# Kernel optimization log

Hardware: AMD Instinct MI355X
Metric: run time of the kernel (lower is better)

Reference implementation:

```python
import jax, jax.numpy as jnp
import numpy as np

B, S, D_MODEL, HEAD_DIM = 8, 2048, 2048, 128
NEG = -1.0e9

def setup_inputs() -> dict:
    key = jax.random.key(0)
    ks = jax.random.split(key, 7)
    scale = 1.0 / np.sqrt(D_MODEL)
    return {
        "hidden_state": jax.random.normal(ks[0], (B, S, D_MODEL), dtype=jnp.float32),
        "Wq": jax.random.normal(ks[1], (D_MODEL, HEAD_DIM), dtype=jnp.float32) * scale,
        "bq": jnp.zeros((HEAD_DIM,), dtype=jnp.float32),
        "Wk": jax.random.normal(ks[2], (D_MODEL, HEAD_DIM), dtype=jnp.float32) * scale,
        "bk": jnp.zeros((HEAD_DIM,), dtype=jnp.float32),
        "Wv": jax.random.normal(ks[3], (D_MODEL, HEAD_DIM), dtype=jnp.float32) * scale,
        "bv": jnp.zeros((HEAD_DIM,), dtype=jnp.float32),
    }

def reference(hidden_state, Wq, bq, Wk, bk, Wv, bv):
    # Projections: [B,S,D] @ [D,H] -> [B,S,H]
    q = hidden_state @ Wq + bq
    k = hidden_state @ Wk + bk
    v = hidden_state @ Wv + bv
    # Scaled dot-product scores: [B,S,S]
    scores = jnp.einsum('bqh,bkh->bqk', q, k) / jnp.sqrt(jnp.float32(HEAD_DIM))
    # Causal mask: strictly-upper-triangular (diagonal kept) gets -1e9, matching
    # band_part(upper) - band_part(diag) in the original.
    S_len = q.shape[1]
    row = jnp.arange(S_len)[:, None]
    col = jnp.arange(S_len)[None, :]
    mask = jnp.where(col > row, jnp.float32(NEG), jnp.float32(0.0))
    scores = scores + mask
    weights = jax.nn.softmax(scores, axis=-1)
    return jnp.einsum('bqk,bkh->bqh', weights, v)
```

## Files before the change

kernel.cpp:

```cpp
#include <hip/hip_runtime.h>
#include <hip/hip_bf16.h>
#include <stdint.h>

#define B_DIM 8
#define S_LEN 2048
#define DMODEL 2048
#define HDIM 128

typedef __attribute__((ext_vector_type(4))) float f32x4;
typedef __attribute__((ext_vector_type(8))) short bf16x8;
typedef __attribute__((ext_vector_type(4))) short bf16x4;
typedef __attribute__((ext_vector_type(4))) unsigned int u32x4;
typedef unsigned short u16;
typedef unsigned int u32;

__device__ __forceinline__ u16 f2bf(float f) {
    union { float f; u32 u; } v; v.f = f;
    u32 u = v.u;
    u32 r = (u + 0x7fffu + ((u >> 16) & 1u)) >> 16;
    return (u16)r;
}

__device__ __forceinline__ u32 pk2bf(float a, float b) {
    float2 f2; f2.x = a; f2.y = b;
    __hip_bfloat162 h = __float22bfloat162_rn(f2);
    union { __hip_bfloat162 h; u32 u; } cv; cv.h = h;
    return cv.u;
}

__device__ __forceinline__ void async_copy16(u16* lds, const u16* g) {
    __builtin_amdgcn_global_load_lds((const __attribute__((address_space(1))) u32*)g,
                                     (__attribute__((address_space(3))) u32*)lds,
                                     16, 0, 0);
}

__global__ void pack_weights(const float* __restrict__ Wq, const float* __restrict__ Wk,
                             const float* __restrict__ Wv, u16* __restrict__ Wp) {
    __shared__ u16 tl[64 * 64];
    int t = threadIdx.x;
    int bx = blockIdx.x;
    int w = bx >> 6;
    int kt = (bx >> 1) & 31;
    int ht = bx & 1;
    int k0 = kt * 64, h0 = ht * 64;
    const float* W = (w == 0) ? Wq : ((w == 1) ? Wk : Wv);

    int kl = t >> 2, hc = t & 3;
    const float* src = W + (size_t)(k0 + kl) * HDIM + h0 + hc * 16;
#pragma unroll
    for (int half = 0; half < 2; half++) {
        bf16x8 p;
#pragma unroll
        for (int j = 0; j < 8; j++) p[j] = (short)f2bf(src[half * 8 + j]);
        int slot = hc * 2 + half;
        *(bf16x8*)((char*)tl + kl * 128 + ((slot ^ (kl & 7)) << 4)) = p;
    }
    __syncthreads();
    int hl = t >> 2, kc = t & 3;
    u16* dst = Wp + (size_t)(w * HDIM + h0 + hl) * DMODEL + k0 + kc * 16;
#pragma unroll
    for (int half = 0; half < 2; half++) {
        bf16x8 p;
#pragma unroll
        for (int j = 0; j < 8; j++) {
            int k = kc * 16 + half * 8 + j;
            p[j] = *(u16*)((char*)tl + k * 128 + (((hl >> 3) ^ (k & 7)) << 4) + (hl & 7) * 2);
        }
        *(bf16x8*)(dst + half * 8) = p;
    }
}

__launch_bounds__(512)
__global__ void qkv_gemm(const float* __restrict__ hs, const u16* __restrict__ Wp,
                         const float* __restrict__ bq, const float* __restrict__ bk,
                         const float* __restrict__ bv,
                         u16* __restrict__ Qb, u16* __restrict__ Kb, u16* __restrict__ Vt) {
    __shared__ u16 As[2][64 * 64];
    __shared__ u16 Bs[2][384 * 64];

    int t = threadIdx.x;
    int wv = t >> 6, l = t & 63, lr = l & 15, lq = l >> 4;
    int wm = wv >> 2, wn = wv & 3;
    int m0 = blockIdx.x * 64;
    int ko = ((blockIdx.x >> 3) & 31) << 6;

#define KW(X) (((X) + ko) & (DMODEL - 1))

    f32x4 acc[2][6] = {};

    int ar = t >> 3, aq = t & 7;
    const float* gA = hs + (size_t)(m0 + ar) * DMODEL + aq * 8;

    f32x4 p0A, p1A, p0B, p1B;

#define STAGE_B(K0, BUF)                                                    \
    {                                                                       \
        _Pragma("unroll")                                                   \
        for (int i = 0; i < 6; i++) {                                       \
            int c = i * 512 + t;                                            \
            int n = c >> 3, s = c & 7;                                      \
            async_copy16(&Bs[BUF][c * 8],                                   \
                         Wp + (size_t)n * DMODEL + (K0) + ((s ^ (n & 7)) * 8)); \
        }                                                                   \
    }
#define WRITE_A(BUF, V0, V1)                                                \
    {                                                                       \
        u32x4 pk;                                                           \
        pk.x = pk2bf(V0[0], V0[1]); pk.y = pk2bf(V0[2], V0[3]);             \
        pk.z = pk2bf(V1[0], V1[1]); pk.w = pk2bf(V1[2], V1[3]);             \
        *(u32x4*)((char*)&As[BUF][0] + ar * 128 + ((aq ^ (ar & 7)) << 4)) = pk; \
    }
#define COMPUTE(CUR)                                                        \
    {                                                                       \
        _Pragma("unroll")                                                   \
        for (int kk = 0; kk < 2; kk++) {                                    \
            bf16x8 afr[2], bfr[6];                                          \
            int slot = kk * 4 + lq;                                         \
            _Pragma("unroll")                                               \
            for (int mi = 0; mi < 2; mi++) {                                \
                int row = wm * 32 + mi * 16 + lr;                           \
                afr[mi] = *(bf16x8*)((char*)&As[CUR][0] + row * 128 + ((slot ^ (row & 7)) << 4)); \
            }                                                               \
            _Pragma("unroll")                                               \
            for (int ni = 0; ni < 6; ni++) {                                \
                int row = wn * 96 + ni * 16 + lr;                           \
                bfr[ni] = *(bf16x8*)((char*)&Bs[CUR][0] + row * 128 + ((slot ^ (row & 7)) << 4)); \
            }                                                               \
            __builtin_amdgcn_s_setprio(1);                                  \
            _Pragma("unroll")                                               \
            for (int mi = 0; mi < 2; mi++)                                  \
                _Pragma("unroll")                                           \
                for (int ni = 0; ni < 6; ni++)                              \
                    acc[mi][ni] = __builtin_amdgcn_mfma_f32_16x16x32_bf16(afr[mi], bfr[ni], acc[mi][ni], 0, 0, 0); \
            __builtin_amdgcn_s_setprio(0);                                  \
        }                                                                   \
    }
#define SYNC_PIPE                                                           \
    asm volatile("s_waitcnt vmcnt(2) lgkmcnt(0)" ::: "memory");             \
    __builtin_amdgcn_sched_barrier(0);                                      \
    __builtin_amdgcn_s_barrier();                                           \
    __builtin_amdgcn_sched_barrier(0);

    p0A = *(const f32x4*)(gA + KW(0)); p1A = *(const f32x4*)(gA + KW(0) + 4);
    STAGE_B(KW(0), 0);
    WRITE_A(0, p0A, p1A);
    p0A = *(const f32x4*)(gA + KW(64)); p1A = *(const f32x4*)(gA + KW(64) + 4);
    __syncthreads();

    for (int k0 = 0; k0 < DMODEL; k0 += 128) {
        {
            int ks = KW(k0 + 64);
            int kp = KW(k0 + 128);
            STAGE_B(ks, 1);
            p0B = *(const f32x4*)(gA + kp); p1B = *(const f32x4*)(gA + kp + 4);
            COMPUTE(0);
            WRITE_A(1, p0A, p1A);
            SYNC_PIPE
        }
        {
            int ks = KW(k0 + 128);
            int kp = KW(k0 + 192);
            STAGE_B(ks, 0);
            p0A = *(const f32x4*)(gA + kp); p1A = *(const f32x4*)(gA + kp + 4);
            COMPUTE(1);
            WRITE_A(0, p0B, p1B);
            SYNC_PIPE
        }
    }

#pragma unroll
    for (int ni = 0; ni < 6; ni++) {
        int col = wn * 96 + ni * 16 + lr;
        int w = col >> 7, h = col & 127;
        const float* bp = (w == 0) ? bq : ((w == 1) ? bk : bv);
        float bias = bp[h];
#pragma unroll
        for (int mi = 0; mi < 2; mi++) {
            int row0 = m0 + wm * 32 + mi * 16 + lq * 4;
            if (w == 2) {
                int b = row0 >> 11, s0 = row0 & (S_LEN - 1);
                bf16x4 pv;
#pragma unroll
                for (int r = 0; r < 4; r++) pv[r] = (short)f2bf(acc[mi][ni][r] + bias);
                *(bf16x4*)(Vt + (size_t)(b * HDIM + h) * S_LEN + s0) = pv;
            } else {
                float scale = (w == 0) ? 0.08838834764831845f : 1.0f;
                u16* dst = (w == 0) ? Qb : Kb;
#pragma unroll
                for (int r = 0; r < 4; r++)
                    dst[(size_t)(row0 + r) * HDIM + h] = f2bf((acc[mi][ni][r] + bias) * scale);
            }
        }
    }
#undef STAGE_B
#undef WRITE_A
#undef COMPUTE
#undef SYNC_PIPE
#undef KW
}

__launch_bounds__(256, 2)
__global__ void attn(const u16* __restrict__ Qb, const u16* __restrict__ Kb,
                     const u16* __restrict__ Vt, float* __restrict__ out) {
    __shared__ char lds[66560];
    float* Om = (float*)lds;
    float* ml = (float*)(lds + 65536);

    int t = threadIdx.x;
    int wv = t >> 6, l = t & 63, lr = l & 15, lq = l >> 4;
    int bx = blockIdx.x;
    int b = bx & 7;
    int qt = 63 - (bx >> 3);
    int qr0 = qt * 32;
    size_t qbase = (size_t)b * S_LEN;
    char* Pw = lds + wv * 16384;

    bf16x8 aqf[2][4];
#pragma unroll
    for (int mi = 0; mi < 2; mi++)
#pragma unroll
        for (int kk = 0; kk < 4; kk++)
            aqf[mi][kk] = *(const bf16x8*)(Qb + (qbase + qr0 + mi * 16 + lr) * HDIM + kk * 32 + lq * 8);

    f32x4 o_acc[2][8] = {};
    float m_run[2][4], l_run[2][4];
#pragma unroll
    for (int mi = 0; mi < 2; mi++)
#pragma unroll
        for (int r = 0; r < 4; r++) { m_run[mi][r] = -1e38f; l_run[mi][r] = 0.f; }

    int ktd = qt >> 1;
    const u16* Kbase = Kb + qbase * HDIM;
    const u16* Vbase = Vt + (size_t)b * HDIM * S_LEN;

    int cnt = (ktd >= wv) ? (((ktd - wv) >> 2) + 1) : 0;

    for (int j = 0; j < cnt; ++j) {
        int kt = wv + (j << 2);
        int kv0 = kt * 64;

        f32x4 sa[2][4] = {};
#pragma unroll
        for (int kk = 0; kk < 4; kk++) {
            bf16x8 bk8[4];
#pragma unroll
            for (int n = 0; n < 4; n++)
                bk8[n] = *(const bf16x8*)(Kbase + (size_t)(kv0 + n * 16 + lr) * HDIM + kk * 32 + lq * 8);
            __builtin_amdgcn_s_setprio(1);
#pragma unroll
            for (int n = 0; n < 4; n++) {
                sa[0][n] = __builtin_amdgcn_mfma_f32_16x16x32_bf16(aqf[0][kk], bk8[n], sa[0][n], 0, 0, 0);
                sa[1][n] = __builtin_amdgcn_mfma_f32_16x16x32_bf16(aqf[1][kk], bk8[n], sa[1][n], 0, 0, 0);
            }
            __builtin_amdgcn_s_setprio(0);
        }

        if (kt == ktd) {
#pragma unroll
            for (int n = 0; n < 4; n++) {
                int col = kv0 + n * 16 + lr;
#pragma unroll
                for (int mi = 0; mi < 2; mi++)
#pragma unroll
                    for (int r = 0; r < 4; r++) {
                        int row = qr0 + mi * 16 + lq * 4 + r;
                        if (col > row) sa[mi][n][r] = -1e30f;
                    }
            }
        }

#pragma unroll
        for (int mi = 0; mi < 2; mi++) {
#pragma unroll
            for (int r = 0; r < 4; r++) {
                float pmx = fmaxf(fmaxf(sa[mi][0][r], sa[mi][1][r]), fmaxf(sa[mi][2][r], sa[mi][3][r]));
                if (__any(pmx > m_run[mi][r] + 8.0f)) {
                    float mx = pmx;
#pragma unroll
                    for (int off = 8; off >= 1; off >>= 1) mx = fmaxf(mx, __shfl_xor(mx, off, 64));
                    float mnew = fmaxf(m_run[mi][r], mx);
                    float f = __expf(m_run[mi][r] - mnew);
                    l_run[mi][r] *= f;
                    m_run[mi][r] = mnew;
#pragma unroll
                    for (int n = 0; n < 8; n++) o_acc[mi][n][r] *= f;
                }
                int prow = mi * 16 + lq * 4 + r;
                char* pb = Pw + prow * 128;
#pragma unroll
                for (int n = 0; n < 4; n++) {
                    float e = __expf(sa[mi][n][r] - m_run[mi][r]);
                    l_run[mi][r] += e;
                    int col = n * 16 + lr;
                    *(u16*)(pb + (((col >> 3) ^ (prow & 7)) << 4) + (col & 7) * 2) = f2bf(e);
                }
            }
        }

#pragma unroll
        for (int kk = 0; kk < 2; kk++) {
            int slot = kk * 4 + lq;
            int row0 = lr, row1 = 16 + lr;
            bf16x8 pa0 = *(bf16x8*)(Pw + row0 * 128 + ((slot ^ (row0 & 7)) << 4));
            bf16x8 pa1 = *(bf16x8*)(Pw + row1 * 128 + ((slot ^ (row1 & 7)) << 4));
            __builtin_amdgcn_s_setprio(1);
#pragma unroll
            for (int n = 0; n < 8; n++) {
                bf16x8 vb8 = *(const bf16x8*)(Vbase + (size_t)(n * 16 + lr) * S_LEN + kv0 + kk * 32 + lq * 8);
                o_acc[0][n] = __builtin_amdgcn_mfma_f32_16x16x32_bf16(pa0, vb8, o_acc[0][n], 0, 0, 0);
                o_acc[1][n] = __builtin_amdgcn_mfma_f32_16x16x32_bf16(pa1, vb8, o_acc[1][n], 0, 0, 0);
            }
            __builtin_amdgcn_s_setprio(0);
        }
    }

#pragma unroll
    for (int mi = 0; mi < 2; mi++)
#pragma unroll
        for (int r = 0; r < 4; r++) {
#pragma unroll
            for (int off = 8; off >= 1; off >>= 1)
                l_run[mi][r] += __shfl_xor(l_run[mi][r], off, 64);
        }

    __builtin_amdgcn_sched_barrier(0);
#pragma unroll
    for (int mi = 0; mi < 2; mi++)
#pragma unroll
        for (int n = 0; n < 8; n++)
#pragma unroll
            for (int r = 0; r < 4; r++)
                Om[wv * 4096 + (mi * 16 + lq * 4 + r) * 128 + n * 16 + lr] = o_acc[mi][n][r];
    if (lr == 0) {
#pragma unroll
        for (int mi = 0; mi < 2; mi++)
#pragma unroll
            for (int r = 0; r < 4; r++) {
                int row = mi * 16 + lq * 4 + r;
                ml[wv * 64 + row * 2 + 0] = m_run[mi][r];
                ml[wv * 64 + row * 2 + 1] = l_run[mi][r];
            }
    }
    __syncthreads();

    {
        int row = t >> 3, c0 = (t & 7) * 16;
        float m4[4], l4[4];
#pragma unroll
        for (int w = 0; w < 4; w++) {
            m4[w] = ml[w * 64 + row * 2 + 0];
            l4[w] = ml[w * 64 + row * 2 + 1];
        }
        float ms = fmaxf(fmaxf(m4[0], m4[1]), fmaxf(m4[2], m4[3]));
        float wt[4], ls = 0.f;
#pragma unroll
        for (int w = 0; w < 4; w++) { wt[w] = __expf(m4[w] - ms); ls += l4[w] * wt[w]; }
        float inv = 1.0f / ls;
        f32x4 r0 = (f32x4)0.f, r1 = (f32x4)0.f, r2 = (f32x4)0.f, r3 = (f32x4)0.f;
#pragma unroll
        for (int w = 0; w < 4; w++) {
            const f32x4* Op = (const f32x4*)(Om + w * 4096 + row * 128 + c0);
            r0 += Op[0] * wt[w];
            r1 += Op[1] * wt[w];
            r2 += Op[2] * wt[w];
            r3 += Op[3] * wt[w];
        }
        f32x4* dst = (f32x4*)(out + (qbase + qr0 + row) * HDIM + c0);
        dst[0] = r0 * inv;
        dst[1] = r1 * inv;
        dst[2] = r2 * inv;
        dst[3] = r3 * inv;
    }
}

extern "C" void kernel_launch(void* const* d_in, const int* in_sizes, int n_in,
                              void* d_out, int out_size, void* d_ws, size_t ws_size,
                              hipStream_t stream) {
    const float* hs = (const float*)d_in[0];
    const float* Wq = (const float*)d_in[1];
    const float* bq = (const float*)d_in[2];
    const float* Wk = (const float*)d_in[3];
    const float* bk = (const float*)d_in[4];
    const float* Wv = (const float*)d_in[5];
    const float* bv = (const float*)d_in[6];
    float* out = (float*)d_out;

    char* ws = (char*)d_ws;
    u16* Qb = (u16*)(ws);
    u16* Kb = (u16*)(ws + (size_t)(4  << 20));
    u16* Vt = (u16*)(ws + (size_t)(8  << 20));
    u16* Wp = (u16*)(ws + (size_t)(12 << 20));

    hipLaunchKernelGGL(pack_weights, dim3(192), dim3(256), 0, stream, Wq, Wk, Wv, Wp);
    hipLaunchKernelGGL(qkv_gemm, dim3(256), dim3(512), 0, stream, hs, Wp, bq, bk, bv, Qb, Kb, Vt);
    hipLaunchKernelGGL(attn, dim3(512), dim3(256), 0, stream, Qb, Kb, Vt, out);
}
```

Before: 108.2 us.

## Split QKV GEMM columns across two blocks and use a triple-buffered pipeline

The QKV projection GEMM now splits its 384 output columns into two 192-column halves, so twice as many blocks are launched (512 instead of 256), each with half the B tile and accumulators. The main loop moves from double to triple buffering: it prefetches two stages ahead with finer-grained vmcnt waits and one barrier per 64-wide K step. The goal is better occupancy across the CUs and more overlap of global loads with MFMA work. The cost is that each block reloads and converts the fp32 hidden-state A tile, so total A traffic and conversion work double.

```diff
diff --git a/kernel.cpp b/kernel.cpp
--- a/kernel.cpp
+++ b/kernel.cpp
@@ -75,102 +75,110 @@
                          const float* __restrict__ bq, const float* __restrict__ bk,
                          const float* __restrict__ bv,
                          u16* __restrict__ Qb, u16* __restrict__ Kb, u16* __restrict__ Vt) {
-    __shared__ u16 As[2][64 * 64];
-    __shared__ u16 Bs[2][384 * 64];
+    __shared__ u16 As[3][64 * 64];
+    __shared__ u16 Bs[3][192 * 64];
 
     int t = threadIdx.x;
     int wv = t >> 6, l = t & 63, lr = l & 15, lq = l >> 4;
     int wm = wv >> 2, wn = wv & 3;
-    int m0 = blockIdx.x * 64;
+    int m0 = (blockIdx.x >> 1) * 64;
+    int col0 = (blockIdx.x & 1) * 192;
     int ko = ((blockIdx.x >> 3) & 31) << 6;
 
 #define KW(X) (((X) + ko) & (DMODEL - 1))
 
-    f32x4 acc[2][6] = {};
+    f32x4 acc[2][3] = {};
 
     int ar = t >> 3, aq = t & 7;
     const float* gA = hs + (size_t)(m0 + ar) * DMODEL + aq * 8;
 
-    f32x4 p0A, p1A, p0B, p1B;
+    f32x4 a0[3], a1[3];
 
 #define STAGE_B(K0, BUF)                                                    \
     {                                                                       \
         _Pragma("unroll")                                                   \
-        for (int i = 0; i < 6; i++) {                                       \
+        for (int i = 0; i < 3; i++) {                                       \
             int c = i * 512 + t;                                            \
             int n = c >> 3, s = c & 7;                                      \
             async_copy16(&Bs[BUF][c * 8],                                   \
-                         Wp + (size_t)n * DMODEL + (K0) + ((s ^ (n & 7)) * 8)); \
+                         Wp + (size_t)(col0 + n) * DMODEL + (K0) + ((s ^ (n & 7)) * 8)); \
         }                                                                   \
     }
-#define WRITE_A(BUF, V0, V1)                                                \
+#define LOAD_A(SET, K)                                                      \
+    { a0[SET] = *(const f32x4*)(gA + (K)); a1[SET] = *(const f32x4*)(gA + (K) + 4); }
+#define WRITE_A(BUF, SET)                                                   \
     {                                                                       \
         u32x4 pk;                                                           \
-        pk.x = pk2bf(V0[0], V0[1]); pk.y = pk2bf(V0[2], V0[3]);             \
-        pk.z = pk2bf(V1[0], V1[1]); pk.w = pk2bf(V1[2], V1[3]);             \
+        pk.x = pk2bf(a0[SET][0], a0[SET][1]); pk.y = pk2bf(a0[SET][2], a0[SET][3]); \
+        pk.z = pk2bf(a1[SET][0], a1[SET][1]); pk.w = pk2bf(a1[SET][2], a1[SET][3]); \
         *(u32x4*)((char*)&As[BUF][0] + ar * 128 + ((aq ^ (ar & 7)) << 4)) = pk; \
     }
-#define COMPUTE(CUR)                                                        \
+#define COMPUTE(J)                                                          \
     {                                                                       \
         _Pragma("unroll")                                                   \
         for (int kk = 0; kk < 2; kk++) {                                    \
-            bf16x8 afr[2], bfr[6];                                          \
+            bf16x8 afr[2], bfr[3];                                          \
             int slot = kk * 4 + lq;                                         \
             _Pragma("unroll")                                               \
             for (int mi = 0; mi < 2; mi++) {                                \
                 int row = wm * 32 + mi * 16 + lr;                           \
-                afr[mi] = *(bf16x8*)((char*)&As[CUR][0] + row * 128 + ((slot ^ (row & 7)) << 4)); \
+                afr[mi] = *(bf16x8*)((char*)&As[J][0] + row * 128 + ((slot ^ (row & 7)) << 4)); \
             }                                                               \
             _Pragma("unroll")                                               \
-            for (int ni = 0; ni < 6; ni++) {                                \
-                int row = wn * 96 + ni * 16 + lr;                           \
-                bfr[ni] = *(bf16x8*)((char*)&Bs[CUR][0] + row * 128 + ((slot ^ (row & 7)) << 4)); \
+            for (int ni = 0; ni < 3; ni++) {                                \
+                int row = wn * 48 + ni * 16 + lr;                           \
+                bfr[ni] = *(bf16x8*)((char*)&Bs[J][0] + row * 128 + ((slot ^ (row & 7)) << 4)); \
             }                                                               \
             __builtin_amdgcn_s_setprio(1);                                  \
             _Pragma("unroll")                                               \
             for (int mi = 0; mi < 2; mi++)                                  \
                 _Pragma("unroll")                                           \
-                for (int ni = 0; ni < 6; ni++)                              \
+                for (int ni = 0; ni < 3; ni++)                              \
                     acc[mi][ni] = __builtin_amdgcn_mfma_f32_16x16x32_bf16(afr[mi], bfr[ni], acc[mi][ni], 0, 0, 0); \
             __builtin_amdgcn_s_setprio(0);                                  \
         }                                                                   \
     }
-#define SYNC_PIPE                                                           \
-    asm volatile("s_waitcnt vmcnt(2) lgkmcnt(0)" ::: "memory");             \
-    __builtin_amdgcn_sched_barrier(0);                                      \
-    __builtin_amdgcn_s_barrier();                                           \
+#define QPHASE(J, K0)                                                       \
+    {                                                                       \
+        int kN = KW((K0) + ((J) + 2) * 64);                                 \
+        STAGE_B(kN, ((J) + 2) % 3);                                         \
+        LOAD_A(((J) + 2) % 3, kN);                                          \
+        __builtin_amdgcn_sched_barrier(0);                                  \
+        asm volatile("s_waitcnt vmcnt(5)" ::: "memory");                    \
+        __builtin_amdgcn_sched_barrier(0);                                  \
+        COMPUTE(J);                                                         \
+        WRITE_A(((J) + 1) % 3, ((J) + 1) % 3);                              \
+        asm volatile("s_waitcnt lgkmcnt(0)" ::: "memory");                  \
+        __builtin_amdgcn_sched_barrier(0);                                  \
+        __builtin_amdgcn_s_barrier();                                       \
+        __builtin_amdgcn_sched_barrier(0);                                  \
+    }
+
+    STAGE_B(KW(0), 0);
+    LOAD_A(0, KW(0));
+    STAGE_B(KW(64), 1);
+    LOAD_A(1, KW(64));
     __builtin_amdgcn_sched_barrier(0);
-
-    p0A = *(const f32x4*)(gA + KW(0)); p1A = *(const f32x4*)(gA + KW(0) + 4);
-    STAGE_B(KW(0), 0);
-    WRITE_A(0, p0A, p1A);
-    p0A = *(const f32x4*)(gA + KW(64)); p1A = *(const f32x4*)(gA + KW(64) + 4);
-    __syncthreads();
-
-    for (int k0 = 0; k0 < DMODEL; k0 += 128) {
-        {
-            int ks = KW(k0 + 64);
-            int kp = KW(k0 + 128);
-            STAGE_B(ks, 1);
-            p0B = *(const f32x4*)(gA + kp); p1B = *(const f32x4*)(gA + kp + 4);
-            COMPUTE(0);
-            WRITE_A(1, p0A, p1A);
-            SYNC_PIPE
-        }
-        {
-            int ks = KW(k0 + 128);
-            int kp = KW(k0 + 192);
-            STAGE_B(ks, 0);
-            p0A = *(const f32x4*)(gA + kp); p1A = *(const f32x4*)(gA + kp + 4);
-            COMPUTE(1);
-            WRITE_A(0, p0B, p1B);
-            SYNC_PIPE
-        }
-    }
-
-#pragma unroll
-    for (int ni = 0; ni < 6; ni++) {
-        int col = wn * 96 + ni * 16 + lr;
+    asm volatile("s_waitcnt vmcnt(5)" ::: "memory");
+    __builtin_amdgcn_sched_barrier(0);
+    WRITE_A(0, 0);
+    asm volatile("s_waitcnt lgkmcnt(0)" ::: "memory");
+    __builtin_amdgcn_sched_barrier(0);
+    __builtin_amdgcn_s_barrier();
+    __builtin_amdgcn_sched_barrier(0);
+
+    for (int it = 0; it < 10; ++it) {
+        int kb = it * 192;
+        QPHASE(0, kb)
+        QPHASE(1, kb)
+        QPHASE(2, kb)
+    }
+    QPHASE(0, 1920)
+    QPHASE(1, 1920)
+
+#pragma unroll
+    for (int ni = 0; ni < 3; ni++) {
+        int col = col0 + wn * 48 + ni * 16 + lr;
         int w = col >> 7, h = col & 127;
         const float* bp = (w == 0) ? bq : ((w == 1) ? bk : bv);
         float bias = bp[h];
@@ -193,9 +201,10 @@
         }
     }
 #undef STAGE_B
+#undef LOAD_A
 #undef WRITE_A
 #undef COMPUTE
-#undef SYNC_PIPE
+#undef QPHASE
 #undef KW
 }
 
@@ -392,6 +401,6 @@
     u16* Wp = (u16*)(ws + (size_t)(12 << 20));
 
     hipLaunchKernelGGL(pack_weights, dim3(192), dim3(256), 0, stream, Wq, Wk, Wv, Wp);
-    hipLaunchKernelGGL(qkv_gemm, dim3(256), dim3(512), 0, stream, hs, Wp, bq, bk, bv, Qb, Kb, Vt);
+    hipLaunchKernelGGL(qkv_gemm, dim3(512), dim3(512), 0, stream, hs, Wp, bq, bk, bv, Qb, Kb, Vt);
     hipLaunchKernelGGL(attn, dim3(512), dim3(256), 0, stream, Qb, Kb, Vt, out);
 }
```

Result: slower. 126.8 us (+17.2%).
